# Kernel tuning notes

Measured on AMD Instinct MI355X. Metric: run time of the kernel, lower is better.

Reference implementation:

```python
import jax, jax.numpy as jnp
import numpy as np

N = 4096      # n_patches / nodes
IN_FEAT = 512
EMBED = 512
HEADS = 8
HEAD_DIM = EMBED // HEADS
SCALING = HEAD_DIM ** -0.5


def setup_inputs() -> dict:
    key = jax.random.key(0)
    ks = jax.random.split(key, 7)
    x = jax.random.normal(ks[0], (N, IN_FEAT), dtype=jnp.float32)
    adj = jax.random.randint(ks[1], (N, N), 0, 2, dtype=jnp.int32)
    s = 0.04  # ~xavier scale for 512x512
    WQ = jax.random.normal(ks[2], (EMBED, IN_FEAT), dtype=jnp.float32) * s
    WK = jax.random.normal(ks[3], (EMBED, IN_FEAT), dtype=jnp.float32) * s
    WV = jax.random.normal(ks[4], (EMBED, IN_FEAT), dtype=jnp.float32) * s
    we = jax.random.normal(ks[5], (1, HEAD_DIM), dtype=jnp.float32) * 0.1
    be = jnp.zeros((1,), dtype=jnp.float32)
    return {"x": x, "adj": adj, "WQ": WQ, "WK": WK, "WV": WV, "we": we, "be": be}


def reference(x, adj, WQ, WK, WV, we, be):
    n = x.shape[0]
    # projections: [N, E] -> [H, N, head_dim]
    Q = (x @ WQ.T).reshape(n, HEADS, HEAD_DIM).transpose(1, 0, 2)
    K = (x @ WK.T).reshape(n, HEADS, HEAD_DIM).transpose(1, 0, 2)
    V = (x @ WV.T).reshape(n, HEADS, HEAD_DIM).transpose(1, 0, 2)
    # scores + per-query energy term: [H, N, N]
    energy = Q @ we.T + be                      # [H, N, 1]
    attn = jnp.einsum('hqd,hkd->hqk', Q, K) * SCALING + energy
    # adjacency mask (broadcast over heads)
    attn = attn + jnp.where(adj > 0, 0.0, -jnp.inf)
    attn = jax.nn.softmax(attn, axis=-1)
    # winner-take-all: one-hot at row max, divided by num_heads
    hard = (attn == jnp.max(attn, axis=-1, keepdims=True)).astype(jnp.float32) / HEADS
    out = jnp.einsum('hqk,hkd->hqd', hard, V)   # [H, N, head_dim]
    return out.transpose(1, 0, 2).reshape(n, EMBED)
```

## Files before the change

kernel.cpp:

```cpp
#include <hip/hip_runtime.h>
#include <hip/hip_bf16.h>
#include <float.h>
#include <stdint.h>

#define NPT    4096
#define EMB    512
#define NH     8
#define HD     64
#define KSPLIT 32

typedef __attribute__((ext_vector_type(8))) short bf16x8;
typedef __attribute__((ext_vector_type(4))) float f32x4;
typedef uint32_t u32;

__device__ __forceinline__ void async_ld16(const void* gsrc, void* ldst) {
    __builtin_amdgcn_global_load_lds(
        (const __attribute__((address_space(1))) u32*)gsrc,
        (__attribute__((address_space(3))) u32*)ldst, 16, 0, 0);
}

__device__ __forceinline__ void split3(float a, unsigned short& h,
                                       unsigned short& m, unsigned short& l) {
    __hip_bfloat16 bh = __float2bfloat16(a);
    float fh = __bfloat162float(bh);
    float r1 = a - fh;
    __hip_bfloat16 bm = __float2bfloat16(r1);
    float fm = __bfloat162float(bm);
    float r2 = r1 - fm;
    __hip_bfloat16 bl = __float2bfloat16(r2);
    h = *reinterpret_cast<unsigned short*>(&bh);
    m = *reinterpret_cast<unsigned short*>(&bm);
    l = *reinterpret_cast<unsigned short*>(&bl);
}

__global__ __launch_bounds__(256) void prep_kernel(const float* __restrict__ x,
                                                   const float* __restrict__ wq,
                                                   const float* __restrict__ wk,
                                                   const float* __restrict__ wv,
                                                   const int* __restrict__ adj,
                                                   unsigned short* __restrict__ xs,
                                                   unsigned short* __restrict__ wqs,
                                                   unsigned short* __restrict__ wks,
                                                   unsigned short* __restrict__ wvs,
                                                   unsigned* __restrict__ bits_t) {
    int y = blockIdx.y;
    size_t i = (size_t)blockIdx.x * 256 + threadIdx.x;
    if (y == 4) {
        int q = (int)(i >> 7), w = (int)i & 127;
        const int4* p = (const int4*)(adj + (size_t)q * NPT + w * 32);
        unsigned m = 0;
#pragma unroll
        for (int j = 0; j < 8; ++j) {
            int4 v = p[j];
            m |= (v.x != 0 ? 1u : 0u) << (j * 4 + 0);
            m |= (v.y != 0 ? 1u : 0u) << (j * 4 + 1);
            m |= (v.z != 0 ? 1u : 0u) << (j * 4 + 2);
            m |= (v.w != 0 ? 1u : 0u) << (j * 4 + 3);
        }
        bits_t[(size_t)w * NPT + q] = m;
    } else if (y == 0) {
        const size_t PL = (size_t)NPT * EMB;
        float4 v = ((const float4*)x)[i];
        ushort4 h, m, l;
        split3(v.x, h.x, m.x, l.x);
        split3(v.y, h.y, m.y, l.y);
        split3(v.z, h.z, m.z, l.z);
        split3(v.w, h.w, m.w, l.w);
        ((ushort4*)xs)[i]            = h;
        ((ushort4*)(xs + PL))[i]     = m;
        ((ushort4*)(xs + 2 * PL))[i] = l;
    } else {
        const size_t WPL = 262144;
        if (i >= WPL / 4) return;
        const float* src = (y == 1) ? wq : (y == 2) ? wk : wv;
        unsigned short* dst = (y == 1) ? wqs : (y == 2) ? wks : wvs;
        float4 v = ((const float4*)src)[i];
        int e  = (int)(i >> 7);
        int k0 = ((int)i & 127) * 4;
        int ebk = e >> 6, el = e & 63;
        int kc = k0 >> 5, g = (k0 >> 3) & 3, dd = k0 & 7;
        size_t off = ((((size_t)ebk * 16 + kc) * 4 + g) * 64 + el) * 8 + dd;
        ushort4 h, m, l;
        split3(v.x, h.x, m.x, l.x);
        split3(v.y, h.y, m.y, l.y);
        split3(v.z, h.z, m.z, l.z);
        split3(v.w, h.w, m.w, l.w);
        *(ushort4*)(dst + off)           = h;
        *(ushort4*)(dst + WPL + off)     = m;
        *(ushort4*)(dst + 2 * WPL + off) = l;
    }
}

__global__ __launch_bounds__(256) void gemm_mfma(const unsigned short* __restrict__ xs,
                                                 const unsigned short* __restrict__ wqs,
                                                 const unsigned short* __restrict__ wks,
                                                 const unsigned short* __restrict__ wvs,
                                                 unsigned short* __restrict__ Q3,
                                                 unsigned short* __restrict__ K3,
                                                 float* __restrict__ V) {
    const int z = blockIdx.z;
    const unsigned short* W3 = (z == 0) ? wqs : (z == 1) ? wks : wvs;
    const size_t XPL = (size_t)NPT * EMB;
    const size_t WPL = 262144;
    const size_t OPL = (size_t)NH * NPT * HD;

    const int nb = blockIdx.x * 128;
    const int ebk = blockIdx.y;
    const int tid = threadIdx.x;
    const int wv = tid >> 6, lane = tid & 63;
    const int m = lane & 15, quad = lane >> 4;
    const int n0 = nb + wv * 32;

    __shared__ __align__(16) unsigned short Ws[2][3 * 2048];

    auto prefetchW = [&](int kc, int buf) {
#pragma unroll
        for (int i2 = 0; i2 < 3; ++i2) {
            int c = wv + 4 * i2;
            int p = c >> 2, sub = c & 3;
            const unsigned short* src = W3 + (size_t)p * WPL
                + ((size_t)ebk * 16 + kc) * 2048 + (sub * 64 + lane) * 8;
            async_ld16(src, &Ws[buf][p * 2048 + sub * 512]);
        }
    };
    bf16x8 bfA[2][3], bfB[2][3];
    auto load_bf = [&](bf16x8 (&bf)[2][3], int kc) {
#pragma unroll
        for (int nt = 0; nt < 2; ++nt)
#pragma unroll
            for (int p = 0; p < 3; ++p)
                bf[nt][p] = *(const bf16x8*)(xs + (size_t)p * XPL
                    + (size_t)(n0 + nt * 16 + m) * EMB + kc * 32 + quad * 8);
    };

    f32x4 acc[4][2];
#pragma unroll
    for (int mt = 0; mt < 4; ++mt)
#pragma unroll
        for (int nt = 0; nt < 2; ++nt) acc[mt][nt] = (f32x4){0.f, 0.f, 0.f, 0.f};

    prefetchW(0, 0);
    load_bf(bfA, 0);

    auto iter = [&](int kc, int buf, bf16x8 (&cur)[2][3], bf16x8 (&nxt)[2][3]) {
        __syncthreads();
        if (kc < 15) { prefetchW(kc + 1, buf ^ 1); load_bf(nxt, kc + 1); }
#pragma unroll
        for (int ga = 0; ga < 3; ++ga) {
            bf16x8 af[4];
#pragma unroll
            for (int mt = 0; mt < 4; ++mt)
                af[mt] = *(const bf16x8*)&Ws[buf][ga * 2048 + (quad * 64 + mt * 16 + m) * 8];
#pragma unroll
            for (int pb = 0; pb < 3 - ga; ++pb)
#pragma unroll
                for (int mt = 0; mt < 4; ++mt)
#pragma unroll
                    for (int nt = 0; nt < 2; ++nt)
                        acc[mt][nt] = __builtin_amdgcn_mfma_f32_16x16x32_bf16(
                            af[mt], cur[nt][pb], acc[mt][nt], 0, 0, 0);
        }
    };

#pragma unroll 1
    for (int kc2 = 0; kc2 < 16; kc2 += 2) {
        iter(kc2, 0, bfA, bfB);
        iter(kc2 + 1, 1, bfB, bfA);
    }

    const int h = ebk;
#pragma unroll
    for (int mt = 0; mt < 4; ++mt)
#pragma unroll
        for (int nt = 0; nt < 2; ++nt) {
            const int n = n0 + nt * 16 + m;
            const int d0 = mt * 16 + quad * 4;
            f32x4 a = acc[mt][nt];
            if (z == 2) {
                *(f32x4*)(V + (size_t)n * EMB + ebk * 64 + d0) = a;
            } else {
                ushort4 ph, pm, pl;
                split3(a[0], ph.x, pm.x, pl.x);
                split3(a[1], ph.y, pm.y, pl.y);
                split3(a[2], ph.z, pm.z, pl.z);
                split3(a[3], ph.w, pm.w, pl.w);
                unsigned short* O3 = (z == 0) ? Q3 : K3;
                size_t off = ((size_t)h * 128 + (n >> 5)) * 2048
                           + (d0 >> 3) * 256 + (n & 31) * 8 + (d0 & 7);
                *(ushort4*)(O3 + off)           = ph;
                *(ushort4*)(O3 + OPL + off)     = pm;
                *(ushort4*)(O3 + 2 * OPL + off) = pl;
            }
        }
}

__global__ __launch_bounds__(256) void score_mfma(const unsigned short* __restrict__ Q3,
                                                  const unsigned short* __restrict__ K3,
                                                  const unsigned* __restrict__ bits_t,
                                                  float* __restrict__ pval,
                                                  int* __restrict__ pidx) {
    const int qb = blockIdx.x * 128;
    const int ks = blockIdx.y;
    const int tid = threadIdx.x;
    const int wv = tid >> 6, lane = tid & 63;
    const int m = lane & 15, quad = lane >> 4;
    const size_t PL = (size_t)NH * NPT * HD;
    const int kq = qb + wv * 32;

    __shared__ __align__(16) unsigned short Ks[3][3 * 2048];

    auto prefetchK = [&](int t) {
        int h = t >> 2, kt = ks * 4 + (t & 3), buf = t % 3;
#pragma unroll
        for (int i2 = 0; i2 < 3; ++i2) {
            int c = wv + 4 * i2;
            int p = c >> 2, sub = c & 3;
            const unsigned short* src = K3 + (size_t)p * PL
                + ((size_t)h * 128 + kt) * 2048 + (sub * 64 + lane) * 8;
            async_ld16(src, &Ks[buf][p * 2048 + sub * 512]);
        }
    };

    prefetchK(0);
    prefetchK(1);

    bf16x8 qf[2][2][3];
    float bestv[2]; int besti[2];

#pragma unroll 1
    for (int t = 0; t < NH * 4; ++t) {
        const int h = t >> 2, kst = t & 3, buf = t % 3;
        const int kbase = ks * 128 + kst * 32;

        asm volatile("s_waitcnt vmcnt(3)\n\ts_barrier" ::: "memory");

        if (kst == 0) {
#pragma unroll
            for (int nt = 0; nt < 2; ++nt)
#pragma unroll
                for (int dc = 0; dc < 2; ++dc)
#pragma unroll
                    for (int p = 0; p < 3; ++p)
                        qf[nt][dc][p] = *(const bf16x8*)(Q3 + (size_t)p * PL
                            + ((size_t)h * 128 + (kq >> 5)) * 2048
                            + (dc * 4 + quad) * 256 + (nt * 16 + m) * 8);
            bestv[0] = bestv[1] = -FLT_MAX;
            besti[0] = besti[1] = 0;
        }

        unsigned bw[2];
#pragma unroll
        for (int nt = 0; nt < 2; ++nt)
            bw[nt] = bits_t[(size_t)(ks * 4 + kst) * NPT + kq + nt * 16 + m];

        if (t + 2 < NH * 4) prefetchK(t + 2);

        f32x4 acc[2][2];
#pragma unroll
        for (int mt = 0; mt < 2; ++mt)
#pragma unroll
            for (int nt = 0; nt < 2; ++nt) acc[mt][nt] = (f32x4){0.f, 0.f, 0.f, 0.f};

#pragma unroll
        for (int ga = 0; ga < 3; ++ga) {
            bf16x8 kf[2][2];
#pragma unroll
            for (int mt = 0; mt < 2; ++mt)
#pragma unroll
                for (int dc = 0; dc < 2; ++dc)
                    kf[mt][dc] = *(const bf16x8*)
                        &Ks[buf][ga * 2048 + ((dc * 4 + quad) * 32 + mt * 16 + m) * 8];
#pragma unroll
            for (int pb = 0; pb < 3 - ga; ++pb)
#pragma unroll
                for (int dc = 0; dc < 2; ++dc)
#pragma unroll
                    for (int mt = 0; mt < 2; ++mt)
#pragma unroll
                        for (int nt = 0; nt < 2; ++nt)
                            acc[mt][nt] = __builtin_amdgcn_mfma_f32_16x16x32_bf16(
                                kf[mt][dc], qf[nt][dc][pb], acc[mt][nt], 0, 0, 0);
        }

#pragma unroll
        for (int nt = 0; nt < 2; ++nt) {
            unsigned w = bw[nt];
#pragma unroll
            for (int mt = 0; mt < 2; ++mt) {
                int k0 = mt * 16 + quad * 4;
                f32x4 a = acc[mt][nt];
#pragma unroll
                for (int r = 0; r < 4; ++r) {
                    if ((w >> (k0 + r)) & 1u) {
                        float s = a[r];
                        if (s > bestv[nt]) { bestv[nt] = s; besti[nt] = kbase + k0 + r; }
                    }
                }
            }
        }

        if (kst == 3) {
#pragma unroll
            for (int nt = 0; nt < 2; ++nt) {
                float v = bestv[nt]; int bi = besti[nt];
#pragma unroll
                for (int off = 16; off < 64; off <<= 1) {
                    float ov = __shfl_xor(v, off);
                    int   oi = __shfl_xor(bi, off);
                    if (ov > v || (ov == v && oi < bi)) { v = ov; bi = oi; }
                }
                if (quad == 0) {
                    size_t o = ((size_t)h * KSPLIT + ks) * NPT + kq + nt * 16 + m;
                    pval[o] = v; pidx[o] = bi;
                }
            }
        }
    }
}

__global__ __launch_bounds__(128) void gather_out(const float* __restrict__ V,
                                                  const float* __restrict__ pval,
                                                  const int* __restrict__ pidx,
                                                  float* __restrict__ out) {
    const int q = blockIdx.x;
    const int tid = threadIdx.x;
    __shared__ int widx[NH];
    if (tid < NH) {
        float bv = -FLT_MAX; int bi = 0;
        for (int ks = 0; ks < KSPLIT; ++ks) {
            size_t off = ((size_t)tid * KSPLIT + ks) * NPT + q;
            float v = pval[off];
            if (v > bv) { bv = v; bi = pidx[off]; }
        }
        widx[tid] = bi;
    }
    __syncthreads();
    const int h = tid >> 4;
    const int d4 = (tid & 15) * 4;
    const int k = widx[h];
    float4 v = *(const float4*)(V + (size_t)k * EMB + h * HD + d4);
    v.x *= 0.125f; v.y *= 0.125f; v.z *= 0.125f; v.w *= 0.125f;
    *(float4*)(out + (size_t)q * EMB + h * HD + d4) = v;
}

extern "C" void kernel_launch(void* const* d_in, const int* in_sizes, int n_in,
                              void* d_out, int out_size, void* d_ws, size_t ws_size,
                              hipStream_t stream) {
    const float* x   = (const float*)d_in[0];
    const int*   adj = (const int*)d_in[1];
    const float* WQ  = (const float*)d_in[2];
    const float* WK  = (const float*)d_in[3];
    const float* WV  = (const float*)d_in[4];
    float* out = (float*)d_out;

    char* ws = (char*)d_ws;
    const size_t HMB = 512u * 1024;
    unsigned short* xs   = (unsigned short*)(ws);
    unsigned short* wqs  = (unsigned short*)(ws + 24 * HMB);
    unsigned short* wks  = (unsigned short*)(ws + 27 * HMB);
    unsigned short* wvs  = (unsigned short*)(ws + 30 * HMB);
    unsigned short* Q3   = (unsigned short*)(ws + 33 * HMB);
    unsigned short* K3   = (unsigned short*)(ws + 57 * HMB);
    float*          V    = (float*)(ws + 81 * HMB);
    unsigned*       bits = (unsigned*)(ws + 97 * HMB);
    float*          pval = (float*)(ws);
    int*            pidx = (int*)(ws + 8 * HMB);

    prep_kernel<<<dim3(2048, 5), dim3(256), 0, stream>>>(x, WQ, WK, WV, adj,
                                                         xs, wqs, wks, wvs, bits);
    gemm_mfma<<<dim3(NPT / 128, NH, 3), dim3(256), 0, stream>>>(xs, wqs, wks, wvs, Q3, K3, V);
    score_mfma<<<dim3(NPT / 128, KSPLIT), dim3(256), 0, stream>>>(Q3, K3, bits, pval, pidx);
    gather_out<<<dim3(NPT), dim3(128), 0, stream>>>(V, pval, pidx, out);
}
```

Before: 279.5 us.

## Replace 3-way bf16 split emulation with 2-way scaled fp16 split

```diff
diff --git a/kernel.cpp b/kernel.cpp
--- a/kernel.cpp
+++ b/kernel.cpp
@@ -9,9 +9,12 @@
 #define HD     64
 #define KSPLIT 32
 
-typedef __attribute__((ext_vector_type(8))) short bf16x8;
+typedef __attribute__((ext_vector_type(8))) _Float16 f16x8;
 typedef __attribute__((ext_vector_type(4))) float f32x4;
 typedef uint32_t u32;
+
+#define LO_SCALE 2048.0f
+#define LO_INV   4.8828125e-4f
 
 __device__ __forceinline__ void async_ld16(const void* gsrc, void* ldst) {
     __builtin_amdgcn_global_load_lds(
@@ -19,18 +22,12 @@
         (__attribute__((address_space(3))) u32*)ldst, 16, 0, 0);
 }
 
-__device__ __forceinline__ void split3(float a, unsigned short& h,
-                                       unsigned short& m, unsigned short& l) {
-    __hip_bfloat16 bh = __float2bfloat16(a);
-    float fh = __bfloat162float(bh);
-    float r1 = a - fh;
-    __hip_bfloat16 bm = __float2bfloat16(r1);
-    float fm = __bfloat162float(bm);
-    float r2 = r1 - fm;
-    __hip_bfloat16 bl = __float2bfloat16(r2);
-    h = *reinterpret_cast<unsigned short*>(&bh);
-    m = *reinterpret_cast<unsigned short*>(&bm);
-    l = *reinterpret_cast<unsigned short*>(&bl);
+__device__ __forceinline__ void split2(float a, unsigned short& h, unsigned short& l) {
+    _Float16 fh = (_Float16)a;
+    float r = (a - (float)fh) * LO_SCALE;
+    _Float16 fl = (_Float16)r;
+    h = *reinterpret_cast<unsigned short*>(&fh);
+    l = *reinterpret_cast<unsigned short*>(&fl);
 }
 
 __global__ __launch_bounds__(256) void prep_kernel(const float* __restrict__ x,
@@ -61,14 +58,13 @@
     } else if (y == 0) {
         const size_t PL = (size_t)NPT * EMB;
         float4 v = ((const float4*)x)[i];
-        ushort4 h, m, l;
-        split3(v.x, h.x, m.x, l.x);
-        split3(v.y, h.y, m.y, l.y);
-        split3(v.z, h.z, m.z, l.z);
-        split3(v.w, h.w, m.w, l.w);
-        ((ushort4*)xs)[i]            = h;
-        ((ushort4*)(xs + PL))[i]     = m;
-        ((ushort4*)(xs + 2 * PL))[i] = l;
+        ushort4 h, l;
+        split2(v.x, h.x, l.x);
+        split2(v.y, h.y, l.y);
+        split2(v.z, h.z, l.z);
+        split2(v.w, h.w, l.w);
+        ((ushort4*)xs)[i]        = h;
+        ((ushort4*)(xs + PL))[i] = l;
     } else {
         const size_t WPL = 262144;
         if (i >= WPL / 4) return;
@@ -80,26 +76,25 @@
         int ebk = e >> 6, el = e & 63;
         int kc = k0 >> 5, g = (k0 >> 3) & 3, dd = k0 & 7;
         size_t off = ((((size_t)ebk * 16 + kc) * 4 + g) * 64 + el) * 8 + dd;
-        ushort4 h, m, l;
-        split3(v.x, h.x, m.x, l.x);
-        split3(v.y, h.y, m.y, l.y);
-        split3(v.z, h.z, m.z, l.z);
-        split3(v.w, h.w, m.w, l.w);
-        *(ushort4*)(dst + off)           = h;
-        *(ushort4*)(dst + WPL + off)     = m;
-        *(ushort4*)(dst + 2 * WPL + off) = l;
+        ushort4 h, l;
+        split2(v.x, h.x, l.x);
+        split2(v.y, h.y, l.y);
+        split2(v.z, h.z, l.z);
+        split2(v.w, h.w, l.w);
+        *(ushort4*)(dst + off)       = h;
+        *(ushort4*)(dst + WPL + off) = l;
     }
 }
 
-__global__ __launch_bounds__(256) void gemm_mfma(const unsigned short* __restrict__ xs,
-                                                 const unsigned short* __restrict__ wqs,
-                                                 const unsigned short* __restrict__ wks,
-                                                 const unsigned short* __restrict__ wvs,
-                                                 unsigned short* __restrict__ Q3,
-                                                 unsigned short* __restrict__ K3,
-                                                 float* __restrict__ V) {
+__global__ __launch_bounds__(256, 3) void gemm_mfma(const unsigned short* __restrict__ xs,
+                                                    const unsigned short* __restrict__ wqs,
+                                                    const unsigned short* __restrict__ wks,
+                                                    const unsigned short* __restrict__ wvs,
+                                                    unsigned short* __restrict__ Q2,
+                                                    unsigned short* __restrict__ K2,
+                                                    float* __restrict__ V) {
     const int z = blockIdx.z;
-    const unsigned short* W3 = (z == 0) ? wqs : (z == 1) ? wks : wvs;
+    const unsigned short* W2 = (z == 0) ? wqs : (z == 1) ? wks : wvs;
     const size_t XPL = (size_t)NPT * EMB;
     const size_t WPL = 262144;
     const size_t OPL = (size_t)NH * NPT * HD;
@@ -111,54 +106,56 @@
     const int m = lane & 15, quad = lane >> 4;
     const int n0 = nb + wv * 32;
 
-    __shared__ __align__(16) unsigned short Ws[2][3 * 2048];
+    __shared__ __align__(16) unsigned short Ws[2][2 * 2048];
 
     auto prefetchW = [&](int kc, int buf) {
 #pragma unroll
-        for (int i2 = 0; i2 < 3; ++i2) {
+        for (int i2 = 0; i2 < 2; ++i2) {
             int c = wv + 4 * i2;
             int p = c >> 2, sub = c & 3;
-            const unsigned short* src = W3 + (size_t)p * WPL
+            const unsigned short* src = W2 + (size_t)p * WPL
                 + ((size_t)ebk * 16 + kc) * 2048 + (sub * 64 + lane) * 8;
             async_ld16(src, &Ws[buf][p * 2048 + sub * 512]);
         }
     };
-    bf16x8 bfA[2][3], bfB[2][3];
-    auto load_bf = [&](bf16x8 (&bf)[2][3], int kc) {
+    f16x8 bfA[2][2], bfB[2][2];
+    auto load_bf = [&](f16x8 (&bf)[2][2], int kc) {
 #pragma unroll
         for (int nt = 0; nt < 2; ++nt)
 #pragma unroll
-            for (int p = 0; p < 3; ++p)
-                bf[nt][p] = *(const bf16x8*)(xs + (size_t)p * XPL
+            for (int p = 0; p < 2; ++p)
+                bf[nt][p] = *(const f16x8*)(xs + (size_t)p * XPL
                     + (size_t)(n0 + nt * 16 + m) * EMB + kc * 32 + quad * 8);
     };
 
-    f32x4 acc[4][2];
-#pragma unroll
-    for (int mt = 0; mt < 4; ++mt)
-#pragma unroll
-        for (int nt = 0; nt < 2; ++nt) acc[mt][nt] = (f32x4){0.f, 0.f, 0.f, 0.f};
+    f32x4 acc[2][4][2];
+#pragma unroll
+    for (int s = 0; s < 2; ++s)
+#pragma unroll
+        for (int mt = 0; mt < 4; ++mt)
+#pragma unroll
+            for (int nt = 0; nt < 2; ++nt) acc[s][mt][nt] = (f32x4){0.f, 0.f, 0.f, 0.f};
 
     prefetchW(0, 0);
     load_bf(bfA, 0);
 
-    auto iter = [&](int kc, int buf, bf16x8 (&cur)[2][3], bf16x8 (&nxt)[2][3]) {
-        __syncthreads();
+    auto iter = [&](int kc, int buf, f16x8 (&cur)[2][2], f16x8 (&nxt)[2][2]) {
+        asm volatile("s_waitcnt vmcnt(4)\n\ts_barrier" ::: "memory");
         if (kc < 15) { prefetchW(kc + 1, buf ^ 1); load_bf(nxt, kc + 1); }
 #pragma unroll
-        for (int ga = 0; ga < 3; ++ga) {
-            bf16x8 af[4];
+        for (int ga = 0; ga < 2; ++ga) {
+            f16x8 af[4];
 #pragma unroll
             for (int mt = 0; mt < 4; ++mt)
-                af[mt] = *(const bf16x8*)&Ws[buf][ga * 2048 + (quad * 64 + mt * 16 + m) * 8];
-#pragma unroll
-            for (int pb = 0; pb < 3 - ga; ++pb)
+                af[mt] = *(const f16x8*)&Ws[buf][ga * 2048 + (quad * 64 + mt * 16 + m) * 8];
+#pragma unroll
+            for (int pb = 0; pb < 2 - ga; ++pb)
 #pragma unroll
                 for (int mt = 0; mt < 4; ++mt)
 #pragma unroll
                     for (int nt = 0; nt < 2; ++nt)
-                        acc[mt][nt] = __builtin_amdgcn_mfma_f32_16x16x32_bf16(
-                            af[mt], cur[nt][pb], acc[mt][nt], 0, 0, 0);
+                        acc[ga + pb][mt][nt] = __builtin_amdgcn_mfma_f32_16x16x32_f16(
+                            af[mt], cur[nt][pb], acc[ga + pb][mt][nt], 0, 0, 0);
         }
     };
 
@@ -175,30 +172,32 @@
         for (int nt = 0; nt < 2; ++nt) {
             const int n = n0 + nt * 16 + m;
             const int d0 = mt * 16 + quad * 4;
-            f32x4 a = acc[mt][nt];
+            f32x4 a;
+#pragma unroll
+            for (int j = 0; j < 4; ++j)
+                a[j] = fmaf(acc[1][mt][nt][j], LO_INV, acc[0][mt][nt][j]);
             if (z == 2) {
                 *(f32x4*)(V + (size_t)n * EMB + ebk * 64 + d0) = a;
             } else {
-                ushort4 ph, pm, pl;
-                split3(a[0], ph.x, pm.x, pl.x);
-                split3(a[1], ph.y, pm.y, pl.y);
-                split3(a[2], ph.z, pm.z, pl.z);
-                split3(a[3], ph.w, pm.w, pl.w);
-                unsigned short* O3 = (z == 0) ? Q3 : K3;
+                ushort4 ph, pl;
+                split2(a[0], ph.x, pl.x);
+                split2(a[1], ph.y, pl.y);
+                split2(a[2], ph.z, pl.z);
+                split2(a[3], ph.w, pl.w);
+                unsigned short* O2 = (z == 0) ? Q2 : K2;
                 size_t off = ((size_t)h * 128 + (n >> 5)) * 2048
                            + (d0 >> 3) * 256 + (n & 31) * 8 + (d0 & 7);
-                *(ushort4*)(O3 + off)           = ph;
-                *(ushort4*)(O3 + OPL + off)     = pm;
-                *(ushort4*)(O3 + 2 * OPL + off) = pl;
+                *(ushort4*)(O2 + off)       = ph;
+                *(ushort4*)(O2 + OPL + off) = pl;
             }
         }
 }
 
-__global__ __launch_bounds__(256) void score_mfma(const unsigned short* __restrict__ Q3,
-                                                  const unsigned short* __restrict__ K3,
-                                                  const unsigned* __restrict__ bits_t,
-                                                  float* __restrict__ pval,
-                                                  int* __restrict__ pidx) {
+__global__ __launch_bounds__(256, 4) void score_mfma(const unsigned short* __restrict__ Q2,
+                                                     const unsigned short* __restrict__ K2,
+                                                     const unsigned* __restrict__ bits_t,
+                                                     float* __restrict__ pval,
+                                                     int* __restrict__ pidx) {
     const int qb = blockIdx.x * 128;
     const int ks = blockIdx.y;
     const int tid = threadIdx.x;
@@ -207,24 +206,37 @@
     const size_t PL = (size_t)NH * NPT * HD;
     const int kq = qb + wv * 32;
 
-    __shared__ __align__(16) unsigned short Ks[3][3 * 2048];
+    __shared__ __align__(16) unsigned short Ks[3][2 * 2048];
 
     auto prefetchK = [&](int t) {
         int h = t >> 2, kt = ks * 4 + (t & 3), buf = t % 3;
 #pragma unroll
-        for (int i2 = 0; i2 < 3; ++i2) {
+        for (int i2 = 0; i2 < 2; ++i2) {
             int c = wv + 4 * i2;
             int p = c >> 2, sub = c & 3;
-            const unsigned short* src = K3 + (size_t)p * PL
+            const unsigned short* src = K2 + (size_t)p * PL
                 + ((size_t)h * 128 + kt) * 2048 + (sub * 64 + lane) * 8;
             async_ld16(src, &Ks[buf][p * 2048 + sub * 512]);
         }
     };
 
+    f16x8 qf[2][2][2];
+    auto load_qf = [&](int hh) {
+#pragma unroll
+        for (int nt = 0; nt < 2; ++nt)
+#pragma unroll
+            for (int dc = 0; dc < 2; ++dc)
+#pragma unroll
+                for (int p = 0; p < 2; ++p)
+                    qf[nt][dc][p] = *(const f16x8*)(Q2 + (size_t)p * PL
+                        + ((size_t)hh * 128 + (kq >> 5)) * 2048
+                        + (dc * 4 + quad) * 256 + (nt * 16 + m) * 8);
+    };
+
+    load_qf(0);
     prefetchK(0);
     prefetchK(1);
 
-    bf16x8 qf[2][2][3];
     float bestv[2]; int besti[2];
 
 #pragma unroll 1
@@ -232,55 +244,46 @@
         const int h = t >> 2, kst = t & 3, buf = t % 3;
         const int kbase = ks * 128 + kst * 32;
 
-        asm volatile("s_waitcnt vmcnt(3)\n\ts_barrier" ::: "memory");
-
-        if (kst == 0) {
-#pragma unroll
-            for (int nt = 0; nt < 2; ++nt)
-#pragma unroll
-                for (int dc = 0; dc < 2; ++dc)
-#pragma unroll
-                    for (int p = 0; p < 3; ++p)
-                        qf[nt][dc][p] = *(const bf16x8*)(Q3 + (size_t)p * PL
-                            + ((size_t)h * 128 + (kq >> 5)) * 2048
-                            + (dc * 4 + quad) * 256 + (nt * 16 + m) * 8);
-            bestv[0] = bestv[1] = -FLT_MAX;
-            besti[0] = besti[1] = 0;
-        }
+        asm volatile("s_waitcnt vmcnt(2)\n\ts_barrier" ::: "memory");
+
+        if (kst == 0) { bestv[0] = bestv[1] = -FLT_MAX; besti[0] = besti[1] = 0; }
 
         unsigned bw[2];
 #pragma unroll
         for (int nt = 0; nt < 2; ++nt)
             bw[nt] = bits_t[(size_t)(ks * 4 + kst) * NPT + kq + nt * 16 + m];
 
+        f32x4 acc[2][2][2];
+#pragma unroll
+        for (int s = 0; s < 2; ++s)
+#pragma unroll
+            for (int mt = 0; mt < 2; ++mt)
+#pragma unroll
+                for (int nt = 0; nt < 2; ++nt) acc[s][mt][nt] = (f32x4){0.f, 0.f, 0.f, 0.f};
+
+#pragma unroll
+        for (int ga = 0; ga < 2; ++ga) {
+            f16x8 kf[2][2];
+#pragma unroll
+            for (int mt = 0; mt < 2; ++mt)
+#pragma unroll
+                for (int dc = 0; dc < 2; ++dc)
+                    kf[mt][dc] = *(const f16x8*)
+                        &Ks[buf][ga * 2048 + ((dc * 4 + quad) * 32 + mt * 16 + m) * 8];
+#pragma unroll
+            for (int pb = 0; pb < 2 - ga; ++pb)
+#pragma unroll
+                for (int dc = 0; dc < 2; ++dc)
+#pragma unroll
+                    for (int mt = 0; mt < 2; ++mt)
+#pragma unroll
+                        for (int nt = 0; nt < 2; ++nt)
+                            acc[ga + pb][mt][nt] = __builtin_amdgcn_mfma_f32_16x16x32_f16(
+                                kf[mt][dc], qf[nt][dc][pb], acc[ga + pb][mt][nt], 0, 0, 0);
+        }
+
+        if (kst == 3 && h + 1 < NH) load_qf(h + 1);
         if (t + 2 < NH * 4) prefetchK(t + 2);
-
-        f32x4 acc[2][2];
-#pragma unroll
-        for (int mt = 0; mt < 2; ++mt)
-#pragma unroll
-            for (int nt = 0; nt < 2; ++nt) acc[mt][nt] = (f32x4){0.f, 0.f, 0.f, 0.f};
-
-#pragma unroll
-        for (int ga = 0; ga < 3; ++ga) {
-            bf16x8 kf[2][2];
-#pragma unroll
-            for (int mt = 0; mt < 2; ++mt)
-#pragma unroll
-                for (int dc = 0; dc < 2; ++dc)
-                    kf[mt][dc] = *(const bf16x8*)
-                        &Ks[buf][ga * 2048 + ((dc * 4 + quad) * 32 + mt * 16 + m) * 8];
-#pragma unroll
-            for (int pb = 0; pb < 3 - ga; ++pb)
-#pragma unroll
-                for (int dc = 0; dc < 2; ++dc)
-#pragma unroll
-                    for (int mt = 0; mt < 2; ++mt)
-#pragma unroll
-                        for (int nt = 0; nt < 2; ++nt)
-                            acc[mt][nt] = __builtin_amdgcn_mfma_f32_16x16x32_bf16(
-                                kf[mt][dc], qf[nt][dc][pb], acc[mt][nt], 0, 0, 0);
-        }
 
 #pragma unroll
         for (int nt = 0; nt < 2; ++nt) {
@@ -288,11 +291,11 @@
 #pragma unroll
             for (int mt = 0; mt < 2; ++mt) {
                 int k0 = mt * 16 + quad * 4;
-                f32x4 a = acc[mt][nt];
+                f32x4 a0 = acc[0][mt][nt], a1 = acc[1][mt][nt];
 #pragma unroll
                 for (int r = 0; r < 4; ++r) {
                     if ((w >> (k0 + r)) & 1u) {
-                        float s = a[r];
+                        float s = fmaf(a1[r], LO_INV, a0[r]);
                         if (s > bestv[nt]) { bestv[nt] = s; besti[nt] = kbase + k0 + r; }
                     }
                 }
@@ -356,19 +359,19 @@
     char* ws = (char*)d_ws;
     const size_t HMB = 512u * 1024;
     unsigned short* xs   = (unsigned short*)(ws);
-    unsigned short* wqs  = (unsigned short*)(ws + 24 * HMB);
-    unsigned short* wks  = (unsigned short*)(ws + 27 * HMB);
-    unsigned short* wvs  = (unsigned short*)(ws + 30 * HMB);
-    unsigned short* Q3   = (unsigned short*)(ws + 33 * HMB);
-    unsigned short* K3   = (unsigned short*)(ws + 57 * HMB);
-    float*          V    = (float*)(ws + 81 * HMB);
-    unsigned*       bits = (unsigned*)(ws + 97 * HMB);
+    unsigned short* wqs  = (unsigned short*)(ws + 16 * HMB);
+    unsigned short* wks  = (unsigned short*)(ws + 18 * HMB);
+    unsigned short* wvs  = (unsigned short*)(ws + 20 * HMB);
+    unsigned short* Q2   = (unsigned short*)(ws + 22 * HMB);
+    unsigned short* K2   = (unsigned short*)(ws + 38 * HMB);
+    float*          V    = (float*)(ws + 54 * HMB);
+    unsigned*       bits = (unsigned*)(ws + 70 * HMB);
     float*          pval = (float*)(ws);
     int*            pidx = (int*)(ws + 8 * HMB);
 
     prep_kernel<<<dim3(2048, 5), dim3(256), 0, stream>>>(x, WQ, WK, WV, adj,
                                                          xs, wqs, wks, wvs, bits);
-    gemm_mfma<<<dim3(NPT / 128, NH, 3), dim3(256), 0, stream>>>(xs, wqs, wks, wvs, Q3, K3, V);
-    score_mfma<<<dim3(NPT / 128, KSPLIT), dim3(256), 0, stream>>>(Q3, K3, bits, pval, pidx);
+    gemm_mfma<<<dim3(NPT / 128, NH, 3), dim3(256), 0, stream>>>(xs, wqs, wks, wvs, Q2, K2, V);
+    score_mfma<<<dim3(NPT / 128, KSPLIT), dim3(256), 0, stream>>>(Q2, K2, bits, pval, pidx);
     gather_out<<<dim3(NPT), dim3(128), 0, stream>>>(V, pval, pidx, out);
 }
```

New measurement: 233.6 us. -16.4%, faster.
